# Optimization experiments

Hardware: AMD Instinct MI355X
Metric: run time of the kernel (lower is better)

The kernel has to match this reference:

```python
import jax, jax.numpy as jnp
import numpy as np

EPS_F = 1e-12
M, N = 64, 4096  # feature dim m, num nodes n


def setup_inputs() -> dict:
    key = jax.random.key(0)
    k1, k2, k3, k4 = jax.random.split(key, 4)
    # X: (m, n) node features transposed, as in the repo (features.t())
    X = jax.random.normal(k1, (M, N), dtype=jnp.float32)
    # F: (m, m) parameter, xavier_uniform init
    bound = float(np.sqrt(6.0 / (M + M)))
    F = jax.random.uniform(k2, (M, M), minval=-bound, maxval=bound, dtype=jnp.float32)
    # Q_S: (n, n) orthogonal eigenvector matrix of the (symmetric, normalized) adjacency
    A = jax.random.normal(k3, (N, N), dtype=jnp.float32)
    Q_S, _ = jnp.linalg.qr(A)
    Q_S = Q_S.astype(jnp.float32)
    # Lambda_S: (n, 1) eigenvalues of normalized adjacency, inside (-1, 1)
    Lambda_S = jnp.sort(
        jax.random.uniform(k4, (N, 1), minval=-0.95, maxval=0.95, dtype=jnp.float32), axis=0
    )
    gamma = jnp.asarray(0.8, dtype=jnp.float32)
    return {"X": X, "F": F, "Q_S": Q_S, "Lambda_S": Lambda_S, "gamma": gamma}


def reference(X, F, Q_S, Lambda_S, gamma):
    # g(F) = F^T F / (||F^T F||_F + eps)  -- Frobenius-normalized Gram matrix
    FF = F.T @ F                                   # (m, m)
    G_F = FF / (jnp.linalg.norm(FF) + EPS_F)       # (m, m), symmetric PSD, ||.||_F ~ 1
    # spectral decomposition of g(F)
    Lambda_F, Q_F = jnp.linalg.eigh(G_F)           # (m,), (m, m)
    # closed-form equilibrium of Z = gamma * g(F) Z S^T + X in the joint eigenbasis
    D = 1.0 / (1.0 - gamma * Lambda_F[:, None] * Lambda_S.reshape(1, -1))  # (m, n)
    Z = Q_F @ (D * (Q_F.T @ X @ Q_S)) @ Q_S.T      # (m, n)
    return Z
```

## Files before the change

### kernel.cpp

```cpp
#include <hip/hip_runtime.h>
#include <math.h>


typedef short short8 __attribute__((ext_vector_type(8)));
typedef float floatx16 __attribute__((ext_vector_type(16)));

#define KSPLIT 32
#define KCHUNK 128
constexpr int Mdim = 64;
constexpr int Ndim = 4096;
constexpr int TILE = Mdim * Ndim;

__device__ inline ushort f2bf(float f) {
    uint u = __float_as_uint(f);
    u += 0x7fff + ((u >> 16) & 1);
    return (ushort)(u >> 16);
}
__device__ inline float bf2f(ushort h) { return __uint_as_float(((uint)h) << 16); }

__device__ inline floatx16 mfma_bf16(short8 a, short8 b, floatx16 c) {
    return __builtin_amdgcn_mfma_f32_32x32x16_bf16(a, b, c, 0, 0, 0);
}

union SharedG1 {
    struct { ushort Ah[4096], Al[4096], Bh[4096]; } g;
    struct { ushort planes[2][4096]; float red[256]; } p;
};

__device__ inline void barrier_nodrain() {
    asm volatile("s_waitcnt lgkmcnt(0)" ::: "memory");
    __builtin_amdgcn_s_barrier();
    __builtin_amdgcn_sched_barrier(0);
}

__device__ void prep_body(SharedG1& sh, const float* __restrict__ F, float* __restrict__ Gout) {
    const int t = threadIdx.x;
    const int l = t & 63, w = t >> 6;
    const int tm = w & 1, tn = w >> 1;
    const int am = tm * 32 + (l & 31);
    const int bn = tn * 32 + (l & 31);
    const int lk = l >> 5;
    ushort* Ph = sh.p.planes[0];
    ushort* Pl = sh.p.planes[1];
    float* red = sh.p.red;

    {
        const int r = t >> 2, c0 = (t & 3) * 16;
#pragma unroll
        for (int q = 0; q < 4; ++q) {
            float4 v = *(const float4*)&F[r * 64 + c0 + 4 * q];
            float fa[4] = {v.x, v.y, v.z, v.w};
#pragma unroll
            for (int i = 0; i < 4; ++i) {
                int c = c0 + 4 * q + i;
                ushort h = f2bf(fa[i]);
                int idx = c * 64 + (((r >> 3) ^ (c & 7)) * 8) + (r & 7);
                Ph[idx] = h;
                Pl[idx] = f2bf(fa[i] - bf2f(h));
            }
        }
    }
    barrier_nodrain();
    floatx16 acc;
    for (int i = 0; i < 16; ++i) acc[i] = 0.f;
    for (int s16 = 0; s16 < 4; ++s16) {
        int gk = 2 * s16 + lk;
        int ai = am * 64 + ((gk ^ (am & 7)) * 8);
        int bi = bn * 64 + ((gk ^ (bn & 7)) * 8);
        short8 ah = *(const short8*)&Ph[ai];
        short8 al = *(const short8*)&Pl[ai];
        short8 bh = *(const short8*)&Ph[bi];
        short8 bl = *(const short8*)&Pl[bi];
        acc = mfma_bf16(ah, bh, acc);
        acc = mfma_bf16(al, bh, acc);
        acc = mfma_bf16(ah, bl, acc);
    }
    float ss = 0.f;
    for (int r = 0; r < 16; ++r) ss += acc[r] * acc[r];
    red[t] = ss;
    barrier_nodrain();
    for (int off = 128; off > 0; off >>= 1) {
        if (t < off) red[t] += red[t + off];
        barrier_nodrain();
    }
    const float inv = 1.0f / (sqrtf(red[0]) + 1e-12f);
    for (int r = 0; r < 16; ++r) {
        int row = (r & 3) + 8 * (r >> 2) + 4 * lk + tm * 32;
        int col = tn * 32 + (l & 31);
        float v = acc[r] * inv;
        Gout[row * 64 + col] = v;
        ushort h = f2bf(v);
        int idx = row * 64 + (((col >> 3) ^ (row & 7)) * 8 + (col & 7));
        Ph[idx] = h;
        Pl[idx] = f2bf(v - bf2f(h));
    }
    for (int j = 1; j < 5; ++j) {
        barrier_nodrain();
        floatx16 a2;
        for (int i = 0; i < 16; ++i) a2[i] = 0.f;
        for (int s16 = 0; s16 < 4; ++s16) {
            int gk = 2 * s16 + lk;
            int ai = am * 64 + ((gk ^ (am & 7)) * 8);
            int bi = bn * 64 + ((gk ^ (bn & 7)) * 8);
            short8 ah = *(const short8*)&Ph[ai];
            short8 al = *(const short8*)&Pl[ai];
            short8 bh = *(const short8*)&Ph[bi];
            short8 bl = *(const short8*)&Pl[bi];
            a2 = mfma_bf16(ah, bh, a2);
            a2 = mfma_bf16(al, bh, a2);
            a2 = mfma_bf16(ah, bl, a2);
        }
        barrier_nodrain();
        for (int r = 0; r < 16; ++r) {
            int row = (r & 3) + 8 * (r >> 2) + 4 * lk + tm * 32;
            int col = tn * 32 + (l & 31);
            float v = a2[r];
            Gout[j * 4096 + row * 64 + col] = v;
            ushort h = f2bf(v);
            int idx = row * 64 + (((col >> 3) ^ (row & 7)) * 8 + (col & 7));
            Ph[idx] = h;
            Pl[idx] = f2bf(v - bf2f(h));
        }
    }
}

template <bool TB>
__device__ inline void load_b(float4 (&dst)[4], const float* __restrict__ Bm,
                              int n0, int kk, int sr, int sj, int nq, int kr2) {
    if constexpr (TB) {
#pragma unroll
        for (int s = 0; s < 4; ++s)
            dst[s] = *(const float4*)&Bm[(size_t)(n0 + sr) * 4096 + kk + 4 * sj + 16 * s];
    } else {
#pragma unroll
        for (int s = 0; s < 2; ++s) {
            dst[2 * s + 0] = *(const float4*)&Bm[(size_t)(kk + kr2 + 32 * s) * 4096 + n0 + 4 * nq];
            dst[2 * s + 1] = *(const float4*)&Bm[(size_t)(kk + kr2 + 1 + 32 * s) * 4096 + n0 + 4 * nq];
        }
    }
}

__global__ __launch_bounds__(256, 4) void gemm1_kernel(const float* __restrict__ A,
                                                       const float* __restrict__ Bm,
                                                       float* __restrict__ C,
                                                       const float* __restrict__ F,
                                                       float* __restrict__ Gp) {
    __shared__ SharedG1 sh;
    const int bid = blockIdx.x;
    if (bid == 0) { prep_body(sh, F, Gp); return; }
    const int b = bid - 1;
    const int n0 = (b & 63) * 64;
    const int ks = b >> 6;
    const int kb = ks * KCHUNK;
    const int t = threadIdx.x;
    const int l = t & 63, w = t >> 6;
    const int tm = w & 1, tn = w >> 1;
    const int am = tm * 32 + (l & 31);
    const int bn = tn * 32 + (l & 31);
    const int lk = l >> 5;
    const int sr = t >> 2, sj = t & 3;
    const int nq = t & 15, kr2 = 2 * (t >> 4);

    floatx16 acc;
    for (int i = 0; i < 16; ++i) acc[i] = 0.f;

    float4 bbuf[2][4];
    load_b<false>(bbuf[0], Bm, n0, kb, sr, sj, nq, kr2);
    load_b<false>(bbuf[1], Bm, n0, kb + 64, sr, sj, nq, kr2);

#pragma unroll
    for (int step = 0; step < KCHUNK / 64; ++step) {
        const int k0 = kb + step * 64;
        float4 av[4];
#pragma unroll
        for (int s = 0; s < 4; ++s)
            av[s] = *(const float4*)&A[sr * 4096 + k0 + 4 * sj + 16 * s];
        barrier_nodrain();
#pragma unroll
        for (int s = 0; s < 2; ++s) {
            int k = kr2 + 32 * s;
            float fa[4] = {bbuf[step][2 * s].x, bbuf[step][2 * s].y, bbuf[step][2 * s].z, bbuf[step][2 * s].w};
            float fb[4] = {bbuf[step][2 * s + 1].x, bbuf[step][2 * s + 1].y, bbuf[step][2 * s + 1].z, bbuf[step][2 * s + 1].w};
#pragma unroll
            for (int i = 0; i < 4; ++i) {
                int n = 4 * nq + i;
                int idx = n * 64 + (((k >> 3) ^ (n & 7)) * 8 + (k & 7));
                ushort2 hp2;
                hp2.x = f2bf(fa[i]);
                hp2.y = f2bf(fb[i]);
                *(ushort2*)&sh.g.Bh[idx] = hp2;
            }
        }
#pragma unroll
        for (int s = 0; s < 4; ++s) {
            int off = 4 * sj + 16 * s;
            int idx = sr * 64 + (((off >> 3) ^ (sr & 7)) * 8 + (off & 7));
            float fa[4] = {av[s].x, av[s].y, av[s].z, av[s].w};
            ushort4 h4, l4;
            ushort* hp = (ushort*)&h4; ushort* lp = (ushort*)&l4;
#pragma unroll
            for (int i = 0; i < 4; ++i) {
                ushort h = f2bf(fa[i]);
                hp[i] = h; lp[i] = f2bf(fa[i] - bf2f(h));
            }
            *(ushort4*)&sh.g.Ah[idx] = h4;
            *(ushort4*)&sh.g.Al[idx] = l4;
        }
        barrier_nodrain();
#pragma unroll
        for (int s16 = 0; s16 < 4; ++s16) {
            int gk = 2 * s16 + lk;
            int ai = am * 64 + ((gk ^ (am & 7)) * 8);
            int bi = bn * 64 + ((gk ^ (bn & 7)) * 8);
            short8 ah = *(const short8*)&sh.g.Ah[ai];
            short8 al = *(const short8*)&sh.g.Al[ai];
            short8 bh = *(const short8*)&sh.g.Bh[bi];
            acc = mfma_bf16(ah, bh, acc);
            acc = mfma_bf16(al, bh, acc);
        }
    }
    float* Cp = C + (size_t)ks * TILE;
    const int colg = n0 + tn * 32 + (l & 31);
#pragma unroll
    for (int r = 0; r < 16; ++r) {
        int row = (r & 3) + 8 * (r >> 2) + 4 * lk + tm * 32;
        Cp[row * 4096 + colg] = acc[r];
    }
}

__global__ __launch_bounds__(256) void solve_kernel(const float* __restrict__ P1,
                                                    const float* __restrict__ Gp,
                                                    const float* __restrict__ lam,
                                                    const float* __restrict__ gammap,
                                                    ushort* __restrict__ Yh,
                                                    ushort* __restrict__ Yl) {
    __shared__ float Gs[64][68];
    __shared__ float T[64][17];
    const int t = threadIdx.x;
    const int c0 = blockIdx.x * 16;
    {
        const int r = t >> 2, q = t & 3;
        float4 a = {0.f, 0.f, 0.f, 0.f};
        for (int s = 0; s < KSPLIT; ++s) {
            const float4 v = *(const float4*)&P1[(size_t)s * TILE + (size_t)r * 4096 + c0 + 4 * q];
            a.x += v.x; a.y += v.y; a.z += v.z; a.w += v.w;
        }
        T[r][4 * q + 0] = a.x;
        T[r][4 * q + 1] = a.y;
        T[r][4 * q + 2] = a.z;
        T[r][4 * q + 3] = a.w;
    }
    const int tx = t & 15;
    const int r4 = (t >> 4) * 4;
    const float a0 = gammap[0] * lam[c0 + tx];
    float s = a0;
    for (int j = 0; j < 5; ++j) {
        __syncthreads();
        for (int e = t; e < 4096; e += 256) Gs[e >> 6][e & 63] = Gp[j * 4096 + e];
        __syncthreads();
        float u0 = 0.f, u1 = 0.f, u2 = 0.f, u3 = 0.f;
#pragma unroll 8
        for (int k = 0; k < 64; ++k) {
            const float tv = T[k][tx];
            const float4 g = *(const float4*)&Gs[k][r4];
            u0 += g.x * tv; u1 += g.y * tv; u2 += g.z * tv; u3 += g.w * tv;
        }
        __syncthreads();
        T[r4 + 0][tx] += s * u0;
        T[r4 + 1][tx] += s * u1;
        T[r4 + 2][tx] += s * u2;
        T[r4 + 3][tx] += s * u3;
        s = s * s;
    }
    __syncthreads();
    for (int e = t; e < 1024; e += 256) {
        const int r = e >> 4, cc = e & 15, col = c0 + cc;
        const float v = T[r][cc];
        const ushort h = f2bf(v);
        const int idx = (col >> 3) * 512 + r * 8 + (col & 7);
        Yh[idx] = h;
        Yl[idx] = f2bf(v - bf2f(h));
    }
}

__global__ __launch_bounds__(256, 4) void gemm2_kernel(const ushort* __restrict__ Yh,
                                                       const ushort* __restrict__ Yl,
                                                       const float* __restrict__ Bm,
                                                       float* __restrict__ C) {
    __shared__ ushort Bhs[2][4096];
    const int b = blockIdx.x;
    const int n0 = (b & 63) * 64;
    const int ks = b >> 6;
    const int kb = ks * KCHUNK;
    const int t = threadIdx.x;
    const int l = t & 63, w = t >> 6;
    const int tm = w & 1, tn = w >> 1;
    const int am = tm * 32 + (l & 31);
    const int bn = tn * 32 + (l & 31);
    const int lk = l >> 5;
    const int sr = t >> 2, sj = t & 3;

    floatx16 acc;
    for (int i = 0; i < 16; ++i) acc[i] = 0.f;

    float4 bbuf[2][4];
    load_b<true>(bbuf[0], Bm, n0, kb, sr, sj, 0, 0);
    load_b<true>(bbuf[1], Bm, n0, kb + 64, sr, sj, 0, 0);

#pragma unroll
    for (int step = 0; step < KCHUNK / 64; ++step) {
        const int k0 = kb + step * 64;
        const int par = step & 1;
        short8 afh[4], afl[4];
#pragma unroll
        for (int s16 = 0; s16 < 4; ++s16) {
            int gk = (k0 >> 3) + 2 * s16 + lk;
            afh[s16] = *(const short8*)&Yh[gk * 512 + am * 8];
            afl[s16] = *(const short8*)&Yl[gk * 512 + am * 8];
        }
#pragma unroll
        for (int s = 0; s < 4; ++s) {
            int off = 4 * sj + 16 * s;
            int idx = sr * 64 + (((off >> 3) ^ (sr & 7)) * 8 + (off & 7));
            float fb[4] = {bbuf[step][s].x, bbuf[step][s].y, bbuf[step][s].z, bbuf[step][s].w};
            ushort4 h4;
            ushort* hp = (ushort*)&h4;
#pragma unroll
            for (int i = 0; i < 4; ++i) hp[i] = f2bf(fb[i]);
            *(ushort4*)&Bhs[par][idx] = h4;
        }
        barrier_nodrain();
#pragma unroll
        for (int s16 = 0; s16 < 4; ++s16) {
            int gk = 2 * s16 + lk;
            int bi = bn * 64 + ((gk ^ (bn & 7)) * 8);
            short8 bh = *(const short8*)&Bhs[par][bi];
            acc = mfma_bf16(afh[s16], bh, acc);
            acc = mfma_bf16(afl[s16], bh, acc);
        }
    }
    float* Cp = C + (size_t)ks * TILE;
    const int colg = n0 + tn * 32 + (l & 31);
#pragma unroll
    for (int r = 0; r < 16; ++r) {
        int row = (r & 3) + 8 * (r >> 2) + 4 * lk + tm * 32;
        Cp[row * 4096 + colg] = acc[r];
    }
}

__global__ __launch_bounds__(256) void reduce_kernel(const float* __restrict__ P,
                                                     float* __restrict__ out) {
    const int i = blockIdx.x * 256 + threadIdx.x;
    float4 a = {0.f, 0.f, 0.f, 0.f};
#pragma unroll
    for (int s = 0; s < KSPLIT; ++s) {
        const float4 v = *(const float4*)&P[(size_t)s * TILE + 4 * i];
        a.x += v.x; a.y += v.y; a.z += v.z; a.w += v.w;
    }
    *(float4*)&out[4 * i] = a;
}

extern "C" void kernel_launch(void* const* d_in, const int* in_sizes, int n_in,
                              void* d_out, int out_size, void* d_ws, size_t ws_size,
                              hipStream_t stream) {
    const float* X     = (const float*)d_in[0];
    const float* F     = (const float*)d_in[1];
    const float* Qs    = (const float*)d_in[2];
    const float* lam   = (const float*)d_in[3];
    const float* gamma = (const float*)d_in[4];
    float* Z = (float*)d_out;

    float* P1 = (float*)d_ws;
    float* P2 = P1 + (size_t)KSPLIT * TILE;
    float* Gp = P2 + (size_t)KSPLIT * TILE;
    ushort* Yh = (ushort*)(Gp + 5 * 4096);
    ushort* Yl = Yh + TILE;

    gemm1_kernel<<<64 * KSPLIT + 1, 256, 0, stream>>>(X, Qs, P1, F, Gp);
    solve_kernel<<<Ndim / 16, 256, 0, stream>>>(P1, Gp, lam, gamma, Yh, Yl);
    gemm2_kernel<<<64 * KSPLIT, 256, 0, stream>>>(Yh, Yl, Qs, P2);
    reduce_kernel<<<256, 256, 0, stream>>>(P2, Z);
}
```

Before: 160.5 us.

## Halve split-K count, prefetch B deeper, fuse final reduction via atomic counter

Halves the split-K factor and doubles the per-block K chunk for both GEMMs, which halves the partial-sum traffic written and re-read, and adds a two-step-ahead register prefetch of Q_S tiles. It removes the separate reduce kernel: in gemm2, the last block to finish each column tile (found with an atomic counter reset by a memset) sums the partials and writes Z. The trade-offs are half as many blocks, so less parallelism, more registers for the prefetch buffers, and an extra memset launch.

```diff
diff --git a/kernel.cpp b/kernel.cpp
--- a/kernel.cpp
+++ b/kernel.cpp
@@ -5,8 +5,8 @@
 typedef short short8 __attribute__((ext_vector_type(8)));
 typedef float floatx16 __attribute__((ext_vector_type(16)));
 
-#define KSPLIT 32
-#define KCHUNK 128
+#define KSPLIT 16
+#define KCHUNK 256
 constexpr int Mdim = 64;
 constexpr int Ndim = 4096;
 constexpr int TILE = Mdim * Ndim;
@@ -164,7 +164,7 @@
     floatx16 acc;
     for (int i = 0; i < 16; ++i) acc[i] = 0.f;
 
-    float4 bbuf[2][4];
+    float4 bbuf[4][4];
     load_b<false>(bbuf[0], Bm, n0, kb, sr, sj, nq, kr2);
     load_b<false>(bbuf[1], Bm, n0, kb + 64, sr, sj, nq, kr2);
 
@@ -175,6 +175,8 @@
 #pragma unroll
         for (int s = 0; s < 4; ++s)
             av[s] = *(const float4*)&A[sr * 4096 + k0 + 4 * sj + 16 * s];
+        if (step + 2 < KCHUNK / 64)
+            load_b<false>(bbuf[step + 2], Bm, n0, k0 + 128, sr, sj, nq, kr2);
         barrier_nodrain();
 #pragma unroll
         for (int s = 0; s < 2; ++s) {
@@ -286,10 +288,14 @@
 __global__ __launch_bounds__(256, 4) void gemm2_kernel(const ushort* __restrict__ Yh,
                                                        const ushort* __restrict__ Yl,
                                                        const float* __restrict__ Bm,
-                                                       float* __restrict__ C) {
+                                                       float* __restrict__ P2,
+                                                       float* __restrict__ Z,
+                                                       uint* __restrict__ cnt) {
     __shared__ ushort Bhs[2][4096];
+    __shared__ uint sOld;
     const int b = blockIdx.x;
-    const int n0 = (b & 63) * 64;
+    const int nt = b & 63;
+    const int n0 = nt * 64;
     const int ks = b >> 6;
     const int kb = ks * KCHUNK;
     const int t = threadIdx.x;
@@ -303,7 +309,7 @@
     floatx16 acc;
     for (int i = 0; i < 16; ++i) acc[i] = 0.f;
 
-    float4 bbuf[2][4];
+    float4 bbuf[3][4];
     load_b<true>(bbuf[0], Bm, n0, kb, sr, sj, 0, 0);
     load_b<true>(bbuf[1], Bm, n0, kb + 64, sr, sj, 0, 0);
 
@@ -311,6 +317,9 @@
     for (int step = 0; step < KCHUNK / 64; ++step) {
         const int k0 = kb + step * 64;
         const int par = step & 1;
+        const int slot = step % 3;
+        if (step + 2 < KCHUNK / 64)
+            load_b<true>(bbuf[(step + 2) % 3], Bm, n0, k0 + 128, sr, sj, 0, 0);
         short8 afh[4], afl[4];
 #pragma unroll
         for (int s16 = 0; s16 < 4; ++s16) {
@@ -322,7 +331,7 @@
         for (int s = 0; s < 4; ++s) {
             int off = 4 * sj + 16 * s;
             int idx = sr * 64 + (((off >> 3) ^ (sr & 7)) * 8 + (off & 7));
-            float fb[4] = {bbuf[step][s].x, bbuf[step][s].y, bbuf[step][s].z, bbuf[step][s].w};
+            float fb[4] = {bbuf[slot][s].x, bbuf[slot][s].y, bbuf[slot][s].z, bbuf[slot][s].w};
             ushort4 h4;
             ushort* hp = (ushort*)&h4;
 #pragma unroll
@@ -339,25 +348,33 @@
             acc = mfma_bf16(afl[s16], bh, acc);
         }
     }
-    float* Cp = C + (size_t)ks * TILE;
+    float* Cp = P2 + (size_t)ks * TILE;
     const int colg = n0 + tn * 32 + (l & 31);
 #pragma unroll
     for (int r = 0; r < 16; ++r) {
         int row = (r & 3) + 8 * (r >> 2) + 4 * lk + tm * 32;
         Cp[row * 4096 + colg] = acc[r];
     }
-}
-
-__global__ __launch_bounds__(256) void reduce_kernel(const float* __restrict__ P,
-                                                     float* __restrict__ out) {
-    const int i = blockIdx.x * 256 + threadIdx.x;
-    float4 a = {0.f, 0.f, 0.f, 0.f};
-#pragma unroll
-    for (int s = 0; s < KSPLIT; ++s) {
-        const float4 v = *(const float4*)&P[(size_t)s * TILE + 4 * i];
-        a.x += v.x; a.y += v.y; a.z += v.z; a.w += v.w;
-    }
-    *(float4*)&out[4 * i] = a;
+    __syncthreads();
+    if (t == 0) {
+        __threadfence();
+        sOld = __hip_atomic_fetch_add(&cnt[nt], 1u, __ATOMIC_ACQ_REL, __HIP_MEMORY_SCOPE_AGENT);
+    }
+    __syncthreads();
+    if (sOld == KSPLIT - 1) {
+        __threadfence();
+        for (int e = t; e < 1024; e += 256) {
+            const int r = e >> 4, cq = e & 15;
+            const size_t off = (size_t)r * 4096 + n0 + 4 * cq;
+            float4 a = {0.f, 0.f, 0.f, 0.f};
+#pragma unroll
+            for (int s = 0; s < KSPLIT; ++s) {
+                const float4 v = *(const float4*)&P2[(size_t)s * TILE + off];
+                a.x += v.x; a.y += v.y; a.z += v.z; a.w += v.w;
+            }
+            *(float4*)&Z[off] = a;
+        }
+    }
 }
 
 extern "C" void kernel_launch(void* const* d_in, const int* in_sizes, int n_in,
@@ -375,9 +392,10 @@
     float* Gp = P2 + (size_t)KSPLIT * TILE;
     ushort* Yh = (ushort*)(Gp + 5 * 4096);
     ushort* Yl = Yh + TILE;
-
+    uint* cnt  = (uint*)(Yl + TILE);
+
+    hipMemsetAsync(cnt, 0, 256, stream);
     gemm1_kernel<<<64 * KSPLIT + 1, 256, 0, stream>>>(X, Qs, P1, F, Gp);
     solve_kernel<<<Ndim / 16, 256, 0, stream>>>(P1, Gp, lam, gamma, Yh, Yl);
-    gemm2_kernel<<<64 * KSPLIT, 256, 0, stream>>>(Yh, Yl, Qs, P2);
-    reduce_kernel<<<256, 256, 0, stream>>>(P2, Z);
-}
+    gemm2_kernel<<<64 * KSPLIT, 256, 0, stream>>>(Yh, Yl, Qs, P2, Z, cnt);
+}
```

Result: slower. 228.6 us (+42.4%).

## Halve split-K partials, prefetch deeper, and store partials in fragment-native layout

Applied to the files above, without the earlier changes.

Split-K factor goes from 32 to 16 with a 256-wide K chunk per block, halving the partial-sum traffic written and re-read by the reductions. The B-operand register prefetch is extended to four stages. The GEMM epilogues now write accumulators in MFMA fragment order, so each lane's stores are contiguous. A separate reduce kernel and a new transposing reduce2z kernel undo that layout. The cost is an extra kernel launch, fewer blocks for parallelism (1024 instead of 2048), and more registers for the larger prefetch buffer.

```diff
diff --git a/kernel.cpp b/kernel.cpp
--- a/kernel.cpp
+++ b/kernel.cpp
@@ -5,8 +5,8 @@
 typedef short short8 __attribute__((ext_vector_type(8)));
 typedef float floatx16 __attribute__((ext_vector_type(16)));
 
-#define KSPLIT 32
-#define KCHUNK 128
+#define KSPLIT 16
+#define KCHUNK 256
 constexpr int Mdim = 64;
 constexpr int Ndim = 4096;
 constexpr int TILE = Mdim * Ndim;
@@ -149,7 +149,8 @@
     const int bid = blockIdx.x;
     if (bid == 0) { prep_body(sh, F, Gp); return; }
     const int b = bid - 1;
-    const int n0 = (b & 63) * 64;
+    const int nt = b & 63;
+    const int n0 = nt * 64;
     const int ks = b >> 6;
     const int kb = ks * KCHUNK;
     const int t = threadIdx.x;
@@ -164,7 +165,7 @@
     floatx16 acc;
     for (int i = 0; i < 16; ++i) acc[i] = 0.f;
 
-    float4 bbuf[2][4];
+    float4 bbuf[4][4];
     load_b<false>(bbuf[0], Bm, n0, kb, sr, sj, nq, kr2);
     load_b<false>(bbuf[1], Bm, n0, kb + 64, sr, sj, nq, kr2);
 
@@ -175,6 +176,8 @@
 #pragma unroll
         for (int s = 0; s < 4; ++s)
             av[s] = *(const float4*)&A[sr * 4096 + k0 + 4 * sj + 16 * s];
+        if (step + 2 < KCHUNK / 64)
+            load_b<false>(bbuf[step + 2], Bm, n0, k0 + 128, sr, sj, nq, kr2);
         barrier_nodrain();
 #pragma unroll
         for (int s = 0; s < 2; ++s) {
@@ -219,16 +222,25 @@
             acc = mfma_bf16(al, bh, acc);
         }
     }
-    float* Cp = C + (size_t)ks * TILE;
-    const int colg = n0 + tn * 32 + (l & 31);
-#pragma unroll
-    for (int r = 0; r < 16; ++r) {
-        int row = (r & 3) + 8 * (r >> 2) + 4 * lk + tm * 32;
-        Cp[row * 4096 + colg] = acc[r];
-    }
-}
-
-__global__ __launch_bounds__(256) void solve_kernel(const float* __restrict__ P1,
+    float* Cp = C + (size_t)ks * TILE + nt * 4096;
+    const int base = w * 1024 + l;
+#pragma unroll
+    for (int r = 0; r < 16; ++r) Cp[base + r * 64] = acc[r];
+}
+
+__global__ __launch_bounds__(256) void reduce_kernel(const float* __restrict__ P,
+                                                     float* __restrict__ out) {
+    const int i = blockIdx.x * 256 + threadIdx.x;
+    float4 a = {0.f, 0.f, 0.f, 0.f};
+#pragma unroll
+    for (int s = 0; s < KSPLIT; ++s) {
+        const float4 v = *(const float4*)&P[(size_t)s * TILE + 4 * i];
+        a.x += v.x; a.y += v.y; a.z += v.z; a.w += v.w;
+    }
+    *(float4*)&out[4 * i] = a;
+}
+
+__global__ __launch_bounds__(256) void solve_kernel(const float* __restrict__ W,
                                                     const float* __restrict__ Gp,
                                                     const float* __restrict__ lam,
                                                     const float* __restrict__ gammap,
@@ -238,17 +250,15 @@
     __shared__ float T[64][17];
     const int t = threadIdx.x;
     const int c0 = blockIdx.x * 16;
-    {
-        const int r = t >> 2, q = t & 3;
-        float4 a = {0.f, 0.f, 0.f, 0.f};
-        for (int s = 0; s < KSPLIT; ++s) {
-            const float4 v = *(const float4*)&P1[(size_t)s * TILE + (size_t)r * 4096 + c0 + 4 * q];
-            a.x += v.x; a.y += v.y; a.z += v.z; a.w += v.w;
-        }
-        T[r][4 * q + 0] = a.x;
-        T[r][4 * q + 1] = a.y;
-        T[r][4 * q + 2] = a.z;
-        T[r][4 * q + 3] = a.w;
+    const int nt = blockIdx.x >> 2;
+    for (int e = t; e < 1024; e += 256) {
+        const int row = e >> 4, cc = e & 15;
+        const int cit = (blockIdx.x & 3) * 16 + cc;
+        const int rr = (row & 3) | (((row >> 3) & 3) << 2);
+        const int lk = (row >> 2) & 1;
+        const int ww = (row >> 5) + 2 * (cit >> 5);
+        const int ll = (cit & 31) + 32 * lk;
+        T[row][cc] = W[nt * 4096 + ww * 1024 + rr * 64 + ll];
     }
     const int tx = t & 15;
     const int r4 = (t >> 4) * 4;
@@ -289,7 +299,8 @@
                                                        float* __restrict__ C) {
     __shared__ ushort Bhs[2][4096];
     const int b = blockIdx.x;
-    const int n0 = (b & 63) * 64;
+    const int nt = b & 63;
+    const int n0 = nt * 64;
     const int ks = b >> 6;
     const int kb = ks * KCHUNK;
     const int t = threadIdx.x;
@@ -303,7 +314,7 @@
     floatx16 acc;
     for (int i = 0; i < 16; ++i) acc[i] = 0.f;
 
-    float4 bbuf[2][4];
+    float4 bbuf[4][4];
     load_b<true>(bbuf[0], Bm, n0, kb, sr, sj, 0, 0);
     load_b<true>(bbuf[1], Bm, n0, kb + 64, sr, sj, 0, 0);
 
@@ -311,6 +322,8 @@
     for (int step = 0; step < KCHUNK / 64; ++step) {
         const int k0 = kb + step * 64;
         const int par = step & 1;
+        if (step + 2 < KCHUNK / 64)
+            load_b<true>(bbuf[step + 2], Bm, n0, k0 + 128, sr, sj, 0, 0);
         short8 afh[4], afl[4];
 #pragma unroll
         for (int s16 = 0; s16 < 4; ++s16) {
@@ -339,25 +352,43 @@
             acc = mfma_bf16(afl[s16], bh, acc);
         }
     }
-    float* Cp = C + (size_t)ks * TILE;
-    const int colg = n0 + tn * 32 + (l & 31);
-#pragma unroll
-    for (int r = 0; r < 16; ++r) {
-        int row = (r & 3) + 8 * (r >> 2) + 4 * lk + tm * 32;
-        Cp[row * 4096 + colg] = acc[r];
-    }
-}
-
-__global__ __launch_bounds__(256) void reduce_kernel(const float* __restrict__ P,
-                                                     float* __restrict__ out) {
-    const int i = blockIdx.x * 256 + threadIdx.x;
+    float* Cp = C + (size_t)ks * TILE + nt * 4096;
+    const int base = w * 1024 + l;
+#pragma unroll
+    for (int r = 0; r < 16; ++r) Cp[base + r * 64] = acc[r];
+}
+
+__global__ __launch_bounds__(256) void reduce2z_kernel(const float* __restrict__ P,
+                                                       float* __restrict__ Z) {
+    __shared__ float a4[2][8][64];
+    const int bid = blockIdx.x;
+    const int nt = bid & 63;
+    const int q = bid >> 6;
+    const int tm = q >> 1;
+    const int rbase = (q & 1) * 8;
+    const int t = threadIdx.x;
+    const int tn = t >> 7, rr = (t >> 4) & 7, lq = t & 15;
+    const size_t off = (size_t)nt * 4096 + (tm + 2 * tn) * 1024 + (rbase + rr) * 64 + 4 * lq;
     float4 a = {0.f, 0.f, 0.f, 0.f};
 #pragma unroll
     for (int s = 0; s < KSPLIT; ++s) {
-        const float4 v = *(const float4*)&P[(size_t)s * TILE + 4 * i];
+        const float4 v = *(const float4*)&P[(size_t)s * TILE + off];
         a.x += v.x; a.y += v.y; a.z += v.z; a.w += v.w;
     }
-    *(float4*)&out[4 * i] = a;
+    *(float4*)&a4[tn][rr][4 * lq] = a;
+    __syncthreads();
+    const int orow = q * 16 + (t >> 4);
+    const int cquad = t & 15;
+    const int lk = (orow >> 2) & 1;
+    const int rr2 = ((orow & 3) | (((orow >> 3) & 3) << 2)) - rbase;
+    float4 o;
+    float* op = (float*)&o;
+#pragma unroll
+    for (int v = 0; v < 4; ++v) {
+        const int col = 4 * cquad + v;
+        op[v] = a4[col >> 5][rr2][(col & 31) + 32 * lk];
+    }
+    *(float4*)&Z[(size_t)orow * 4096 + nt * 64 + 4 * cquad] = o;
 }
 
 extern "C" void kernel_launch(void* const* d_in, const int* in_sizes, int n_in,
@@ -372,12 +403,14 @@
 
     float* P1 = (float*)d_ws;
     float* P2 = P1 + (size_t)KSPLIT * TILE;
-    float* Gp = P2 + (size_t)KSPLIT * TILE;
+    float* W  = P2 + (size_t)KSPLIT * TILE;
+    float* Gp = W + TILE;
     ushort* Yh = (ushort*)(Gp + 5 * 4096);
     ushort* Yl = Yh + TILE;
 
     gemm1_kernel<<<64 * KSPLIT + 1, 256, 0, stream>>>(X, Qs, P1, F, Gp);
-    solve_kernel<<<Ndim / 16, 256, 0, stream>>>(P1, Gp, lam, gamma, Yh, Yl);
+    reduce_kernel<<<256, 256, 0, stream>>>(P1, W);
+    solve_kernel<<<Ndim / 16, 256, 0, stream>>>(W, Gp, lam, gamma, Yh, Yl);
     gemm2_kernel<<<64 * KSPLIT, 256, 0, stream>>>(Yh, Yl, Qs, P2);
-    reduce_kernel<<<256, 256, 0, stream>>>(P2, Z);
-}
+    reduce2z_kernel<<<256, 256, 0, stream>>>(P2, Z);
+}
```

New measurement: 158.5 us. No clear change (-1.3%).
